# Performance work log

Hardware: AMD Instinct MI355X
Metric: run time of the kernel (lower is better)

The kernel has to match this reference:

```python
import jax, jax.numpy as jnp
import numpy as np


def setup_inputs() -> dict:
    key = jax.random.key(0)
    k1, k2, k3, k4, k5 = jax.random.split(key, 5)
    N, T, D, H = 64, 512, 512, 512
    std = 1.0 / np.sqrt(H)
    return {
        "x": jax.random.normal(k1, (N, T, D), dtype=jnp.float32),
        "weight_xh": jax.random.uniform(k2, (D, 4 * H), jnp.float32, -std, std),
        "weight_hh": jax.random.uniform(k3, (H, 4 * H), jnp.float32, -std, std),
        "bias_xh": jax.random.uniform(k4, (4 * H,), jnp.float32, -std, std),
        "bias_hh": jax.random.uniform(k5, (4 * H,), jnp.float32, -std, std),
    }


def reference(x, weight_xh, weight_hh, bias_xh, bias_hh):
    # x: (N, T, D) -> (T, N, D)
    x = jnp.transpose(x, (1, 0, 2))
    T, N, _ = x.shape
    H = weight_hh.shape[0]
    # Input projection for all timesteps at once: (T, N, 4H)
    xh = jnp.einsum("tnd,dk->tnk", x, weight_xh) + bias_xh

    def step(carry, xh_t):
        h_prev, c_prev = carry
        gates = xh_t + h_prev @ weight_hh + bias_hh  # (N, 4H)
        i = jax.nn.sigmoid(gates[:, 0:H])
        f = jax.nn.sigmoid(gates[:, H:2 * H])
        g = jnp.tanh(gates[:, 2 * H:3 * H])
        o = jax.nn.sigmoid(gates[:, 3 * H:4 * H])
        c = f * c_prev + i * g
        h = o * jnp.tanh(c)
        return (h, c), h

    h0 = jnp.zeros((N, H), dtype=x.dtype)
    c0 = jnp.zeros((N, H), dtype=x.dtype)
    _, y = jax.lax.scan(step, (h0, c0), xh)  # y: (T, N, H)
    return jnp.transpose(y, (1, 0, 2))  # (N, T, H)
```

## Files before the change

kernel.cpp:

```cpp
#include <hip/hip_runtime.h>

typedef unsigned short u16;
typedef unsigned int   u32;
typedef unsigned long long u64;
typedef __attribute__((ext_vector_type(8))) short short8;
typedef __attribute__((ext_vector_type(4))) float f32x4;
typedef __attribute__((ext_vector_type(2))) unsigned long long u64x2;

#define NB   64
#define TS   512
#define HD   512
#define RG   4
#define CG   32
#define NBLK (RG*CG)
#define HP   130

__device__ __forceinline__ u16 f2bf(float x) {
    union { float f; u32 i; } v; v.f = x;
    u32 r = (v.i + 0x7fffu + ((v.i >> 16) & 1u)) >> 16;
    return (u16)r;
}
__device__ __forceinline__ u32 pack2bf(float a, float b) {
    return (u32)f2bf(a) | ((u32)f2bf(b) << 16);
}
__device__ __forceinline__ float sigmf(float x) { return 1.0f / (1.0f + __expf(-x)); }
__device__ __forceinline__ float tanhf_fast(float x) { return 1.0f - 2.0f / (__expf(2.0f * x) + 1.0f); }

__global__ void cvt_x_k(const float* __restrict__ in, u16* __restrict__ out, int n) {
    int i = (blockIdx.x * blockDim.x + threadIdx.x) * 8;
    const int stride = gridDim.x * blockDim.x * 8;
    for (; i < n; i += stride) {
        const f32x4 a = *(const f32x4*)(in + i);
        const f32x4 b = *(const f32x4*)(in + i + 4);
        u32 q[4];
        q[0] = pack2bf(a[0], a[1]);
        q[1] = pack2bf(a[2], a[3]);
        q[2] = pack2bf(b[0], b[1]);
        q[3] = pack2bf(b[2], b[3]);
        *(f32x4*)(out + i) = *(f32x4*)q;
    }
}

__global__ void transpose_cvt_k(const float* __restrict__ in, u16* __restrict__ out,
                                int R, int C) {
    __shared__ float tile[32][33];
    const int c0 = blockIdx.x * 32;
    const int r0 = blockIdx.y * 32;
    const int tx = threadIdx.x & 31;
    const int ty = threadIdx.x >> 5;
#pragma unroll
    for (int i = 0; i < 32; i += 8)
        tile[ty + i][tx] = in[(size_t)(r0 + ty + i) * C + c0 + tx];
    __syncthreads();
#pragma unroll
    for (int i = 0; i < 32; i += 8)
        out[(size_t)(c0 + ty + i) * R + r0 + tx] = f2bf(tile[tx][ty + i]);
}

__global__ __launch_bounds__(256, 1) void lstm_fused(
    const u16*   __restrict__ xbg,
    const u16*   __restrict__ WtX,
    const u16*   __restrict__ WtH,
    const float* __restrict__ bxh,
    const float* __restrict__ bhh,
    u64*   __restrict__ hbuf,
    float* __restrict__ y,
    u32*   __restrict__ flags)
{
    const int bid  = blockIdx.x;
    const int r    = bid & 3;
    const int cg   = bid >> 2;
    const int tid  = threadIdx.x;
    const int lane = tid & 63;
    const int wv   = tid >> 6;
    const int m15  = lane & 15;
    const int kq   = lane >> 4;
    const int n0   = r * 16;
    const int gcol0 = wv * 512 + cg * 16;

    __shared__ u64   ldsH[16 * HP];
    __shared__ float gbuf[4][16][17];
    __shared__ u16   ht[16][16];

    short8 wx[16], wh[16];
    {
        const u16* px = WtX + (size_t)(gcol0 + m15) * 512 + kq * 8;
        const u16* ph = WtH + (size_t)(gcol0 + m15) * 512 + kq * 8;
#pragma unroll
        for (int kc = 0; kc < 16; ++kc) {
            wx[kc] = *(const short8*)(px + kc * 32);
            wh[kc] = *(const short8*)(ph + kc * 32);
        }
    }
    const float bsum = bxh[gcol0 + m15] + bhh[gcol0 + m15];

    const int erow = tid >> 4;
    const int ecol = tid & 15;
    const int en   = n0 + erow;
    const int hcol = cg * 16 + ecol;
    float cst = 0.0f;

    const int lrow = 4 * wv + (lane >> 4);
    const int c0   = (lane & 15) * 8;

    short8 xb[16];
    {
        const u16* xg = xbg + ((size_t)(n0 + m15) * TS + 0) * HD + kq * 8;
#pragma unroll
        for (int kc = 0; kc < 16; ++kc)
            xb[kc] = *(const short8*)(xg + kc * 32);
    }

    for (int t = 0; t < TS; ++t) {
        u64 hq[8];
        if (t > 0) {
            const u32* fl = flags + (size_t)(t - 1) * (RG * CG) + r * CG;
            u32 v;
            do {
                v = __hip_atomic_load(fl + (lane & 31), __ATOMIC_RELAXED,
                                      __HIP_MEMORY_SCOPE_AGENT);
            } while (!__all(v != 0u));

            const u64* gsrc = hbuf + (size_t)((t - 1) & 3) * (NB * 128)
                            + (size_t)(n0 + lrow) * 128 + c0;
#pragma unroll
            for (int i = 0; i < 8; ++i)
                hq[i] = __hip_atomic_load(gsrc + i, __ATOMIC_RELAXED,
                                          __HIP_MEMORY_SCOPE_AGENT);
        }

        f32x4 a0 = {0.f,0.f,0.f,0.f}, a1 = {0.f,0.f,0.f,0.f};
        f32x4 a2 = {0.f,0.f,0.f,0.f}, a3 = {0.f,0.f,0.f,0.f};
#pragma unroll
        for (int kc = 0; kc < 4; ++kc) {
            a0 = __builtin_amdgcn_mfma_f32_16x16x32_bf16(xb[4*kc + 0], wx[4*kc + 0], a0, 0, 0, 0);
            a1 = __builtin_amdgcn_mfma_f32_16x16x32_bf16(xb[4*kc + 1], wx[4*kc + 1], a1, 0, 0, 0);
            a2 = __builtin_amdgcn_mfma_f32_16x16x32_bf16(xb[4*kc + 2], wx[4*kc + 2], a2, 0, 0, 0);
            a3 = __builtin_amdgcn_mfma_f32_16x16x32_bf16(xb[4*kc + 3], wx[4*kc + 3], a3, 0, 0, 0);
        }

        if (t > 0) {
            u64* ldst = &ldsH[lrow * HP + c0];
            *(u64x2*)(ldst)     = (u64x2){hq[0], hq[1]};
            *(u64x2*)(ldst + 2) = (u64x2){hq[2], hq[3]};
            *(u64x2*)(ldst + 4) = (u64x2){hq[4], hq[5]};
            *(u64x2*)(ldst + 6) = (u64x2){hq[6], hq[7]};
            __syncthreads();

            const u16* lh = (const u16*)ldsH + m15 * (HP * 4) + kq * 8;
#pragma unroll
            for (int kc = 0; kc < 4; ++kc) {
                short8 h0 = *(const short8*)(lh + (4*kc + 0) * 32);
                short8 h1 = *(const short8*)(lh + (4*kc + 1) * 32);
                short8 h2 = *(const short8*)(lh + (4*kc + 2) * 32);
                short8 h3 = *(const short8*)(lh + (4*kc + 3) * 32);
                a0 = __builtin_amdgcn_mfma_f32_16x16x32_bf16(h0, wh[4*kc + 0], a0, 0, 0, 0);
                a1 = __builtin_amdgcn_mfma_f32_16x16x32_bf16(h1, wh[4*kc + 1], a1, 0, 0, 0);
                a2 = __builtin_amdgcn_mfma_f32_16x16x32_bf16(h2, wh[4*kc + 2], a2, 0, 0, 0);
                a3 = __builtin_amdgcn_mfma_f32_16x16x32_bf16(h3, wh[4*kc + 3], a3, 0, 0, 0);
            }
        }

        {
            f32x4 g4 = a0 + a1 + a2 + a3;
#pragma unroll
            for (int j = 0; j < 4; ++j)
                gbuf[wv][kq * 4 + j][m15] = g4[j] + bsum;
        }
        __syncthreads();

        {
            const float gi = gbuf[0][erow][ecol];
            const float gf = gbuf[1][erow][ecol];
            const float gg = gbuf[2][erow][ecol];
            const float go = gbuf[3][erow][ecol];
            const float iv = sigmf(gi);
            const float fv = sigmf(gf);
            const float gv = tanhf_fast(gg);
            const float ov = sigmf(go);
            cst = fv * cst + iv * gv;
            const float hv = ov * tanhf_fast(cst);
            y[((size_t)en * 512 + t) * 512 + hcol] = hv;
            ht[erow][ecol] = f2bf(hv);
        }
        __syncthreads();

        if (tid < 64) {
            const int row = tid >> 2;
            const int c4  = tid & 3;
            const u64 v = *(const u64*)&ht[row][c4 * 4];
            __hip_atomic_store(hbuf + (size_t)(t & 3) * (NB * 128)
                               + (size_t)(n0 + row) * 128 + cg * 4 + c4, v,
                               __ATOMIC_RELAXED, __HIP_MEMORY_SCOPE_AGENT);
        }
        __syncthreads();

        if (t < TS - 1 && tid == 0) {
            __hip_atomic_store(flags + (size_t)t * (RG * CG) + r * CG + cg, 1u,
                               __ATOMIC_RELAXED, __HIP_MEMORY_SCOPE_AGENT);
        }

        if (t + 1 < TS) {
            const u16* xg = xbg + ((size_t)(n0 + m15) * TS + (t + 1)) * HD + kq * 8;
#pragma unroll
            for (int kc = 0; kc < 16; ++kc)
                xb[kc] = *(const short8*)(xg + kc * 32);
        }
    }
}

extern "C" void kernel_launch(void* const* d_in, const int* in_sizes, int n_in,
                              void* d_out, int out_size, void* d_ws, size_t ws_size,
                              hipStream_t stream) {
    const float* x   = (const float*)d_in[0];
    const float* wxh = (const float*)d_in[1];
    const float* whh = (const float*)d_in[2];
    const float* bxh = (const float*)d_in[3];
    const float* bhh = (const float*)d_in[4];
    float* y = (float*)d_out;

    char* ws = (char*)d_ws;
    u32* flags = (u32*)ws;
    u64* hbuf  = (u64*)(ws + (size_t)(1 << 18));
    u16* WtX   = (u16*)(ws + (size_t)(2 << 18));
    u16* WtH   = (u16*)(ws + (size_t)(2 << 18) + (size_t)2048 * 512 * 2);
    u16* xbg   = (u16*)(ws + (size_t)(2 << 18) + (size_t)2 * 2048 * 512 * 2);

    (void)hipMemsetAsync(flags, 0, (size_t)TS * RG * CG * sizeof(u32), stream);

    cvt_x_k<<<2048, 256, 0, stream>>>(x, xbg, NB * TS * HD);

    dim3 tgrid(2048 / 32, 512 / 32);
    transpose_cvt_k<<<tgrid, 256, 0, stream>>>(wxh, WtX, 512, 2048);
    transpose_cvt_k<<<tgrid, 256, 0, stream>>>(whh, WtH, 512, 2048);

    lstm_fused<<<dim3(NBLK), dim3(256), 0, stream>>>(xbg, WtX, WtH, bxh, bhh,
                                                     hbuf, y, flags);
}
```

Baseline: 2.131 ms.

## Replace flag barrier with tagged h-exchange and split K across 512-thread blocks

Replaces the per-timestep flag array and spin-wait with tagged 64-bit hidden-state words: each word carries the timestep in its low half, so consumers poll the data directly and need no separate flag store or extra barriers. The grid is halved to 64 blocks of 512 threads, each covering 32 hidden columns, with the K dimension split across two wave groups and reduced through shared memory. Shared-memory staging of h uses an XOR swizzle to cut bank conflicts. This removes a round trip and two syncthreads per step, at the cost of doubled hbuf traffic from tag bits and more per-block work.

```diff
diff --git a/kernel.cpp b/kernel.cpp
--- a/kernel.cpp
+++ b/kernel.cpp
@@ -5,15 +5,15 @@
 typedef unsigned long long u64;
 typedef __attribute__((ext_vector_type(8))) short short8;
 typedef __attribute__((ext_vector_type(4))) float f32x4;
-typedef __attribute__((ext_vector_type(2))) unsigned long long u64x2;
 
 #define NB   64
 #define TS   512
 #define HD   512
 #define RG   4
-#define CG   32
+#define CG   16
 #define NBLK (RG*CG)
-#define HP   130
+#define HROW 256
+#define SLOT (NB*HROW)
 
 __device__ __forceinline__ u16 f2bf(float x) {
     union { float f; u32 i; } v; v.f = x;
@@ -57,15 +57,14 @@
         out[(size_t)(c0 + ty + i) * R + r0 + tx] = f2bf(tile[tx][ty + i]);
 }
 
-__global__ __launch_bounds__(256, 1) void lstm_fused(
+__global__ __launch_bounds__(512, 2) void lstm_fused(
     const u16*   __restrict__ xbg,
     const u16*   __restrict__ WtX,
     const u16*   __restrict__ WtH,
     const float* __restrict__ bxh,
     const float* __restrict__ bhh,
     u64*   __restrict__ hbuf,
-    float* __restrict__ y,
-    u32*   __restrict__ flags)
+    float* __restrict__ y)
 {
     const int bid  = blockIdx.x;
     const int r    = bid & 3;
@@ -73,138 +72,139 @@
     const int tid  = threadIdx.x;
     const int lane = tid & 63;
     const int wv   = tid >> 6;
+    const int g    = wv & 3;
+    const int kh   = wv >> 2;
     const int m15  = lane & 15;
     const int kq   = lane >> 4;
     const int n0   = r * 16;
-    const int gcol0 = wv * 512 + cg * 16;
-
-    __shared__ u64   ldsH[16 * HP];
-    __shared__ float gbuf[4][16][17];
-    __shared__ u16   ht[16][16];
-
-    short8 wx[16], wh[16];
+    const int gcol0 = g * 512 + cg * 32;
+    const int kbase = kh * 256;
+
+    __shared__ __align__(16) u32 ldsH[16 * 256];
+    __shared__ float gbuf2[2][4][16][34];
+
+    short8 wx[2][8], wh[2][8];
+#pragma unroll
+    for (int c = 0; c < 2; ++c) {
+        const u16* px = WtX + (size_t)(gcol0 + c * 16 + m15) * 512 + kbase + kq * 8;
+        const u16* ph = WtH + (size_t)(gcol0 + c * 16 + m15) * 512 + kbase + kq * 8;
+#pragma unroll
+        for (int kc = 0; kc < 8; ++kc) {
+            wx[c][kc] = *(const short8*)(px + kc * 32);
+            wh[c][kc] = *(const short8*)(ph + kc * 32);
+        }
+    }
+
+    const int erow = tid >> 5;
+    const int ecol = tid & 31;
+    const int hcol = cg * 32 + ecol;
+    const float bI = bxh[hcol]        + bhh[hcol];
+    const float bF = bxh[512  + hcol] + bhh[512  + hcol];
+    const float bG = bxh[1024 + hcol] + bhh[1024 + hcol];
+    const float bO = bxh[1536 + hcol] + bhh[1536 + hcol];
+    float cst = 0.0f;
+
+    const int lrow = 2 * wv + (lane >> 5);
+    const int lq   = lane & 31;
+    const int swzw = (lrow & 7) << 2;
+
+    short8 xb[8];
     {
-        const u16* px = WtX + (size_t)(gcol0 + m15) * 512 + kq * 8;
-        const u16* ph = WtH + (size_t)(gcol0 + m15) * 512 + kq * 8;
-#pragma unroll
-        for (int kc = 0; kc < 16; ++kc) {
-            wx[kc] = *(const short8*)(px + kc * 32);
-            wh[kc] = *(const short8*)(ph + kc * 32);
-        }
-    }
-    const float bsum = bxh[gcol0 + m15] + bhh[gcol0 + m15];
-
-    const int erow = tid >> 4;
-    const int ecol = tid & 15;
-    const int en   = n0 + erow;
-    const int hcol = cg * 16 + ecol;
-    float cst = 0.0f;
-
-    const int lrow = 4 * wv + (lane >> 4);
-    const int c0   = (lane & 15) * 8;
-
-    short8 xb[16];
-    {
-        const u16* xg = xbg + ((size_t)(n0 + m15) * TS + 0) * HD + kq * 8;
-#pragma unroll
-        for (int kc = 0; kc < 16; ++kc)
-            xb[kc] = *(const short8*)(xg + kc * 32);
+        const u16* xg = xbg + (size_t)(n0 + m15) * TS * HD + kbase + kq * 8;
+#pragma unroll
+        for (int kc = 0; kc < 8; ++kc) xb[kc] = *(const short8*)(xg + kc * 32);
     }
 
     for (int t = 0; t < TS; ++t) {
         u64 hq[8];
+        const u64* gsrc = hbuf + (size_t)((t - 1) & 3) * SLOT
+                        + (size_t)(n0 + lrow) * HROW + lq;
         if (t > 0) {
-            const u32* fl = flags + (size_t)(t - 1) * (RG * CG) + r * CG;
-            u32 v;
-            do {
-                v = __hip_atomic_load(fl + (lane & 31), __ATOMIC_RELAXED,
-                                      __HIP_MEMORY_SCOPE_AGENT);
-            } while (!__all(v != 0u));
-
-            const u64* gsrc = hbuf + (size_t)((t - 1) & 3) * (NB * 128)
-                            + (size_t)(n0 + lrow) * 128 + c0;
 #pragma unroll
             for (int i = 0; i < 8; ++i)
-                hq[i] = __hip_atomic_load(gsrc + i, __ATOMIC_RELAXED,
+                hq[i] = __hip_atomic_load(gsrc + i * 32, __ATOMIC_RELAXED,
                                           __HIP_MEMORY_SCOPE_AGENT);
         }
 
-        f32x4 a0 = {0.f,0.f,0.f,0.f}, a1 = {0.f,0.f,0.f,0.f};
-        f32x4 a2 = {0.f,0.f,0.f,0.f}, a3 = {0.f,0.f,0.f,0.f};
-#pragma unroll
-        for (int kc = 0; kc < 4; ++kc) {
-            a0 = __builtin_amdgcn_mfma_f32_16x16x32_bf16(xb[4*kc + 0], wx[4*kc + 0], a0, 0, 0, 0);
-            a1 = __builtin_amdgcn_mfma_f32_16x16x32_bf16(xb[4*kc + 1], wx[4*kc + 1], a1, 0, 0, 0);
-            a2 = __builtin_amdgcn_mfma_f32_16x16x32_bf16(xb[4*kc + 2], wx[4*kc + 2], a2, 0, 0, 0);
-            a3 = __builtin_amdgcn_mfma_f32_16x16x32_bf16(xb[4*kc + 3], wx[4*kc + 3], a3, 0, 0, 0);
+        f32x4 a00 = {0.f,0.f,0.f,0.f}, a01 = {0.f,0.f,0.f,0.f};
+        f32x4 a10 = {0.f,0.f,0.f,0.f}, a11 = {0.f,0.f,0.f,0.f};
+#pragma unroll
+        for (int kc = 0; kc < 8; kc += 2) {
+            a00 = __builtin_amdgcn_mfma_f32_16x16x32_bf16(xb[kc],   wx[0][kc],   a00, 0, 0, 0);
+            a10 = __builtin_amdgcn_mfma_f32_16x16x32_bf16(xb[kc],   wx[1][kc],   a10, 0, 0, 0);
+            a01 = __builtin_amdgcn_mfma_f32_16x16x32_bf16(xb[kc+1], wx[0][kc+1], a01, 0, 0, 0);
+            a11 = __builtin_amdgcn_mfma_f32_16x16x32_bf16(xb[kc+1], wx[1][kc+1], a11, 0, 0, 0);
         }
 
         if (t > 0) {
-            u64* ldst = &ldsH[lrow * HP + c0];
-            *(u64x2*)(ldst)     = (u64x2){hq[0], hq[1]};
-            *(u64x2*)(ldst + 2) = (u64x2){hq[2], hq[3]};
-            *(u64x2*)(ldst + 4) = (u64x2){hq[4], hq[5]};
-            *(u64x2*)(ldst + 6) = (u64x2){hq[6], hq[7]};
+            const u32 tagv = (u32)t;
+            for (;;) {
+                u32 stale = 0;
+#pragma unroll
+                for (int i = 0; i < 8; ++i) stale |= ((u32)hq[i]) ^ tagv;
+                if (__all(stale == 0)) break;
+                __builtin_amdgcn_s_sleep(1);
+#pragma unroll
+                for (int i = 0; i < 8; ++i)
+                    hq[i] = __hip_atomic_load(gsrc + i * 32, __ATOMIC_RELAXED,
+                                              __HIP_MEMORY_SCOPE_AGENT);
+            }
+#pragma unroll
+            for (int i = 0; i < 8; ++i)
+                ldsH[lrow * 256 + ((i * 32 + lq) ^ swzw)] = (u32)(hq[i] >> 32);
             __syncthreads();
 
-            const u16* lh = (const u16*)ldsH + m15 * (HP * 4) + kq * 8;
-#pragma unroll
-            for (int kc = 0; kc < 4; ++kc) {
-                short8 h0 = *(const short8*)(lh + (4*kc + 0) * 32);
-                short8 h1 = *(const short8*)(lh + (4*kc + 1) * 32);
-                short8 h2 = *(const short8*)(lh + (4*kc + 2) * 32);
-                short8 h3 = *(const short8*)(lh + (4*kc + 3) * 32);
-                a0 = __builtin_amdgcn_mfma_f32_16x16x32_bf16(h0, wh[4*kc + 0], a0, 0, 0, 0);
-                a1 = __builtin_amdgcn_mfma_f32_16x16x32_bf16(h1, wh[4*kc + 1], a1, 0, 0, 0);
-                a2 = __builtin_amdgcn_mfma_f32_16x16x32_bf16(h2, wh[4*kc + 2], a2, 0, 0, 0);
-                a3 = __builtin_amdgcn_mfma_f32_16x16x32_bf16(h3, wh[4*kc + 3], a3, 0, 0, 0);
+            const u32* lbase = ldsH + m15 * 256;
+            const int swzr = (m15 & 7) << 2;
+#pragma unroll
+            for (int kc = 0; kc < 8; kc += 2) {
+                short8 h0 = *(const short8*)(lbase + (((kbase >> 1) + kc * 16 + kq * 4) ^ swzr));
+                short8 h1 = *(const short8*)(lbase + (((kbase >> 1) + (kc + 1) * 16 + kq * 4) ^ swzr));
+                a00 = __builtin_amdgcn_mfma_f32_16x16x32_bf16(h0, wh[0][kc],   a00, 0, 0, 0);
+                a10 = __builtin_amdgcn_mfma_f32_16x16x32_bf16(h0, wh[1][kc],   a10, 0, 0, 0);
+                a01 = __builtin_amdgcn_mfma_f32_16x16x32_bf16(h1, wh[0][kc+1], a01, 0, 0, 0);
+                a11 = __builtin_amdgcn_mfma_f32_16x16x32_bf16(h1, wh[1][kc+1], a11, 0, 0, 0);
             }
         }
 
         {
-            f32x4 g4 = a0 + a1 + a2 + a3;
-#pragma unroll
-            for (int j = 0; j < 4; ++j)
-                gbuf[wv][kq * 4 + j][m15] = g4[j] + bsum;
+            const f32x4 s0 = a00 + a01;
+            const f32x4 s1 = a10 + a11;
+#pragma unroll
+            for (int j = 0; j < 4; ++j) {
+                gbuf2[kh][g][kq * 4 + j][m15]      = s0[j];
+                gbuf2[kh][g][kq * 4 + j][16 + m15] = s1[j];
+            }
         }
         __syncthreads();
 
         {
-            const float gi = gbuf[0][erow][ecol];
-            const float gf = gbuf[1][erow][ecol];
-            const float gg = gbuf[2][erow][ecol];
-            const float go = gbuf[3][erow][ecol];
+            const float gi = gbuf2[0][0][erow][ecol] + gbuf2[1][0][erow][ecol] + bI;
+            const float gf = gbuf2[0][1][erow][ecol] + gbuf2[1][1][erow][ecol] + bF;
+            const float gg = gbuf2[0][2][erow][ecol] + gbuf2[1][2][erow][ecol] + bG;
+            const float go = gbuf2[0][3][erow][ecol] + gbuf2[1][3][erow][ecol] + bO;
             const float iv = sigmf(gi);
             const float fv = sigmf(gf);
             const float gv = tanhf_fast(gg);
             const float ov = sigmf(go);
             cst = fv * cst + iv * gv;
             const float hv = ov * tanhf_fast(cst);
-            y[((size_t)en * 512 + t) * 512 + hcol] = hv;
-            ht[erow][ecol] = f2bf(hv);
-        }
-        __syncthreads();
-
-        if (tid < 64) {
-            const int row = tid >> 2;
-            const int c4  = tid & 3;
-            const u64 v = *(const u64*)&ht[row][c4 * 4];
-            __hip_atomic_store(hbuf + (size_t)(t & 3) * (NB * 128)
-                               + (size_t)(n0 + row) * 128 + cg * 4 + c4, v,
-                               __ATOMIC_RELAXED, __HIP_MEMORY_SCOPE_AGENT);
-        }
-        __syncthreads();
-
-        if (t < TS - 1 && tid == 0) {
-            __hip_atomic_store(flags + (size_t)t * (RG * CG) + r * CG + cg, 1u,
-                               __ATOMIC_RELAXED, __HIP_MEMORY_SCOPE_AGENT);
+            y[((size_t)(n0 + erow) * TS + t) * HD + hcol] = hv;
+
+            const u32 me = (u32)f2bf(hv);
+            const u32 nb = (u32)__shfl_xor((int)me, 1);
+            if ((ecol & 1) == 0) {
+                const u64 v = ((u64)(me | (nb << 16)) << 32) | (u64)(u32)(t + 1);
+                __hip_atomic_store(hbuf + (size_t)(t & 3) * SLOT
+                                   + (size_t)(n0 + erow) * HROW + cg * 16 + (ecol >> 1),
+                                   v, __ATOMIC_RELAXED, __HIP_MEMORY_SCOPE_AGENT);
+            }
         }
 
         if (t + 1 < TS) {
-            const u16* xg = xbg + ((size_t)(n0 + m15) * TS + (t + 1)) * HD + kq * 8;
-#pragma unroll
-            for (int kc = 0; kc < 16; ++kc)
-                xb[kc] = *(const short8*)(xg + kc * 32);
+            const u16* xg = xbg + ((size_t)(n0 + m15) * TS + (t + 1)) * HD + kbase + kq * 8;
+#pragma unroll
+            for (int kc = 0; kc < 8; ++kc) xb[kc] = *(const short8*)(xg + kc * 32);
         }
     }
 }
@@ -220,13 +220,12 @@
     float* y = (float*)d_out;
 
     char* ws = (char*)d_ws;
-    u32* flags = (u32*)ws;
-    u64* hbuf  = (u64*)(ws + (size_t)(1 << 18));
-    u16* WtX   = (u16*)(ws + (size_t)(2 << 18));
-    u16* WtH   = (u16*)(ws + (size_t)(2 << 18) + (size_t)2048 * 512 * 2);
-    u16* xbg   = (u16*)(ws + (size_t)(2 << 18) + (size_t)2 * 2048 * 512 * 2);
-
-    (void)hipMemsetAsync(flags, 0, (size_t)TS * RG * CG * sizeof(u32), stream);
+    u64* hbuf = (u64*)ws;
+    u16* WtX  = (u16*)(ws + (size_t)(1 << 19));
+    u16* WtH  = (u16*)(ws + (size_t)(1 << 19) + (size_t)2048 * 512 * 2);
+    u16* xbg  = (u16*)(ws + (size_t)(1 << 19) + (size_t)2 * 2048 * 512 * 2);
+
+    (void)hipMemsetAsync(hbuf, 0, (size_t)4 * SLOT * sizeof(u64), stream);
 
     cvt_x_k<<<2048, 256, 0, stream>>>(x, xbg, NB * TS * HD);
 
@@ -234,6 +233,6 @@
     transpose_cvt_k<<<tgrid, 256, 0, stream>>>(wxh, WtX, 512, 2048);
     transpose_cvt_k<<<tgrid, 256, 0, stream>>>(whh, WtH, 512, 2048);
 
-    lstm_fused<<<dim3(NBLK), dim3(256), 0, stream>>>(xbg, WtX, WtH, bxh, bhh,
-                                                     hbuf, y, flags);
-}
+    lstm_fused<<<dim3(NBLK), dim3(512), 0, stream>>>(xbg, WtX, WtH, bxh, bhh,
+                                                     hbuf, y);
+}
```

Measured after the change: 1.957 ms. 8.2% less time.
